# Kernel optimization log

Measured on AMD Instinct MI355X. Metric: run time of the kernel, lower is better.

Reference implementation:

```python
import jax, jax.numpy as jnp
import numpy as np

HIDDEN = 4096
N_HEADS = 32
N_KV_HEADS = 8
HEAD_DIM = HIDDEN // N_HEADS
KV_GROUPS = N_HEADS // N_KV_HEADS
TEMPERATURE = 1.0
NEG_INF = -1e9


def _bitlinear(x, W):
    """BitNet b1.58 BitLinear: per-token int8 activation quant + ternary weight quant (quant-dequant)."""
    # activation: absmax int8 per last dim
    a_scale = 127.0 / jnp.clip(jnp.max(jnp.abs(x), axis=-1, keepdims=True), 1e-5, None)
    xq = jnp.clip(jnp.round(x * a_scale), -128.0, 127.0) / a_scale
    # weight: ternary with mean-abs scale
    w_scale = jnp.clip(jnp.mean(jnp.abs(W)), 1e-5, None)
    Wq = jnp.clip(jnp.round(W / w_scale), -1.0, 1.0) * w_scale
    return jnp.einsum('bsh,oh->bso', xq, Wq)


def _base2_softmax(x, temperature=TEMPERATURE):
    # numerically stable 2^x softmax: 2^((x-m)/T) / sum
    m = jnp.max(x, axis=-1, keepdims=True)
    p = jnp.exp2((x - m) / temperature)
    return p / jnp.sum(p, axis=-1, keepdims=True)


def setup_inputs() -> dict:
    key = jax.random.key(0)
    ks = jax.random.split(key, 6)
    B, S = 2, 2048
    hidden_states = jax.random.normal(ks[0], (B, S, HIDDEN), dtype=jnp.float32)
    # additive causal mask [B, 1, S, S]
    causal = jnp.tril(jnp.ones((S, S), dtype=bool))
    attention_mask = jnp.where(causal, 0.0, NEG_INF).astype(jnp.float32)[None, None]
    attention_mask = jnp.broadcast_to(attention_mask, (B, 1, S, S))
    Wq = jax.random.normal(ks[1], (HIDDEN, HIDDEN), dtype=jnp.float32) * 0.02
    Wk = jax.random.normal(ks[2], (N_KV_HEADS * HEAD_DIM, HIDDEN), dtype=jnp.float32) * 0.02
    Wv = jax.random.normal(ks[3], (N_KV_HEADS * HEAD_DIM, HIDDEN), dtype=jnp.float32) * 0.02
    Wo = jax.random.normal(ks[4], (HIDDEN, HIDDEN), dtype=jnp.float32) * 0.02
    return {"hidden_states": hidden_states, "attention_mask": attention_mask,
            "Wq": Wq, "Wk": Wk, "Wv": Wv, "Wo": Wo}


def reference(hidden_states, attention_mask, Wq, Wk, Wv, Wo):
    B, S, _ = hidden_states.shape
    q = _bitlinear(hidden_states, Wq).reshape(B, S, N_HEADS, HEAD_DIM).transpose(0, 2, 1, 3)
    k = _bitlinear(hidden_states, Wk).reshape(B, S, N_KV_HEADS, HEAD_DIM).transpose(0, 2, 1, 3)
    v = _bitlinear(hidden_states, Wv).reshape(B, S, N_KV_HEADS, HEAD_DIM).transpose(0, 2, 1, 3)
    # GQA: repeat each kv head KV_GROUPS times along head dim
    k = jnp.repeat(k, KV_GROUPS, axis=1)
    v = jnp.repeat(v, KV_GROUPS, axis=1)
    attn_weights = jnp.einsum('bhqd,bhkd->bhqk', q, k) / np.sqrt(HEAD_DIM).astype(np.float32)
    attn_weights = attn_weights + attention_mask
    attn_weights = _base2_softmax(attn_weights)
    attn_output = jnp.einsum('bhqk,bhkd->bhqd', attn_weights, v)
    attn_output = attn_output.transpose(0, 2, 1, 3).reshape(B, S, HIDDEN)
    return _bitlinear(attn_output, Wo)
```

## Files before the change

### kernel.cpp

```cpp
#include <hip/hip_runtime.h>
#include <stdint.h>


typedef float  f32x4 __attribute__((ext_vector_type(4)));
typedef short  s16x8 __attribute__((ext_vector_type(8)));
typedef int    i32x4 __attribute__((ext_vector_type(4)));

__device__ __forceinline__ uint16_t f2b(float f) {
  uint32_t u = __float_as_uint(f);
  return (uint16_t)((u + 0x7FFFu + ((u >> 16) & 1u)) >> 16);
}
__device__ __forceinline__ void gl_lds16(const void* g, void* l) {
  __builtin_amdgcn_global_load_lds((const __attribute__((address_space(1))) unsigned int*)g,
                                   (__attribute__((address_space(3))) unsigned int*)l, 16, 0, 0);
}
__device__ __forceinline__ f32x4 mfma_bf16(s16x8 a, s16x8 b, f32x4 c) {
  return __builtin_amdgcn_mfma_f32_16x16x32_bf16(a, b, c, 0, 0, 0);
}
__device__ __forceinline__ i32x4 mfma_i8(i32x4 a, i32x4 b, i32x4 c) {
  return __builtin_amdgcn_mfma_i32_16x16x64_i8(a, b, c, 0, 0, 0);
}

__global__ __launch_bounds__(256) void k_qact_f32(const float* __restrict__ x,
                                                  int8_t* __restrict__ xq, float* __restrict__ rs) {
  __shared__ float red[4];
  const int row = blockIdx.x, t = threadIdx.x;
  const float4* xr = (const float4*)(x + (size_t)row * 4096);
  float v[16];
  #pragma unroll
  for (int i = 0; i < 4; i++) {
    float4 f = xr[t + 256 * i];
    v[i*4+0] = f.x; v[i*4+1] = f.y; v[i*4+2] = f.z; v[i*4+3] = f.w;
  }
  float mx = 0.f;
  #pragma unroll
  for (int i = 0; i < 16; i++) mx = fmaxf(mx, fabsf(v[i]));
  for (int o = 1; o < 64; o <<= 1) mx = fmaxf(mx, __shfl_xor(mx, o));
  if ((t & 63) == 0) red[t >> 6] = mx;
  __syncthreads();
  mx = fmaxf(fmaxf(red[0], red[1]), fmaxf(red[2], red[3]));
  mx = fmaxf(mx, 1e-5f);
  const float a = 127.f / mx;
  if (t == 0) rs[row] = mx * (1.f / 127.f);
  uint32_t* dst = (uint32_t*)(xq + (size_t)row * 4096);
  #pragma unroll
  for (int i = 0; i < 4; i++) {
    uint32_t w = 0;
    #pragma unroll
    for (int j = 0; j < 4; j++) {
      float q = rintf(v[i*4+j] * a);
      q = fmaxf(-128.f, fminf(127.f, q));
      w |= ((uint32_t)((int)q & 255)) << (j * 8);
    }
    dst[t + 256 * i] = w;
  }
}

__global__ __launch_bounds__(256) void k_abssum_part(const float* __restrict__ wq, const float* __restrict__ wk,
                                                     const float* __restrict__ wv, const float* __restrict__ wo,
                                                     double* __restrict__ part) {
  __shared__ double red[4];
  const int blk = blockIdx.x, t = threadIdx.x;
  const float* src; size_t base;
  if (blk < 1024)      { src = wq; base = (size_t)blk * 16384; }
  else if (blk < 1280) { src = wk; base = (size_t)(blk - 1024) * 16384; }
  else if (blk < 1536) { src = wv; base = (size_t)(blk - 1280) * 16384; }
  else                 { src = wo; base = (size_t)(blk - 1536) * 16384; }
  double s = 0.0;
  #pragma unroll
  for (int r = 0; r < 16; r++) {
    float4 f = *(const float4*)(src + base + r * 1024 + t * 4);
    s += (double)fabsf(f.x) + (double)fabsf(f.y) + (double)fabsf(f.z) + (double)fabsf(f.w);
  }
  for (int o = 1; o < 64; o <<= 1) s += __shfl_xor(s, o);
  if ((t & 63) == 0) red[t >> 6] = s;
  __syncthreads();
  if (t == 0) part[blk] = red[0] + red[1] + red[2] + red[3];
}

__global__ __launch_bounds__(256) void k_reduce_sums(const double* __restrict__ part, double* __restrict__ sums) {
  const int w = threadIdx.x >> 6, lane = threadIdx.x & 63;
  const int s0 = (w == 0) ? 0 : (w == 1) ? 1024 : (w == 2) ? 1280 : 1536;
  const int s1 = (w == 0) ? 1024 : (w == 1) ? 1280 : (w == 2) ? 1536 : 2560;
  double s = 0.0;
  for (int i = s0 + lane; i < s1; i += 64) s += part[i];
  for (int o = 1; o < 64; o <<= 1) s += __shfl_xor(s, o);
  if (lane == 0) sums[w] = s;
}

__global__ __launch_bounds__(256) void k_quant_w_all(const float* __restrict__ wq, const float* __restrict__ wk,
                                                     const float* __restrict__ wv, const float* __restrict__ wo,
                                                     int8_t* __restrict__ wqkv, int8_t* __restrict__ woq,
                                                     const double* __restrict__ sums) {
  const int blk = blockIdx.x, t = threadIdx.x;
  const float* src; int8_t* dst; size_t base; int sidx; double ivn;
  if (blk < 1024)      { src = wq; dst = wqkv;                        base = (size_t)blk * 16384;          sidx = 0; ivn = 1.0 / 16777216.0; }
  else if (blk < 1280) { src = wk; dst = wqkv + (size_t)4096 * 4096;  base = (size_t)(blk - 1024) * 16384; sidx = 1; ivn = 1.0 / 4194304.0;  }
  else if (blk < 1536) { src = wv; dst = wqkv + (size_t)5120 * 4096;  base = (size_t)(blk - 1280) * 16384; sidx = 2; ivn = 1.0 / 4194304.0;  }
  else                 { src = wo; dst = woq;                         base = (size_t)(blk - 1536) * 16384; sidx = 3; ivn = 1.0 / 16777216.0; }
  const float ws = (float)fmax(sums[sidx] * ivn, 1e-5);
  #pragma unroll
  for (int r = 0; r < 16; r++) {
    size_t e = base + r * 1024 + t * 4;
    float4 f = *(const float4*)(src + e);
    float hv[4] = {f.x, f.y, f.z, f.w};
    uint32_t w = 0;
    #pragma unroll
    for (int j = 0; j < 4; j++) {
      float q = rintf(hv[j] / ws);
      q = fmaxf(-1.f, fminf(1.f, q));
      w |= ((uint32_t)((int)q & 255)) << (j * 8);
    }
    *(uint32_t*)(dst + e) = w;
  }
}

template<int MODE>
__global__ __launch_bounds__(256) void k_gemm_i8(const int8_t* __restrict__ A, const int8_t* __restrict__ Bw,
                                                 const float* __restrict__ rs, const double* __restrict__ sums,
                                                 uint16_t* __restrict__ qb, uint16_t* __restrict__ kb,
                                                 uint16_t* __restrict__ vb, float* __restrict__ outp) {
  __shared__ int8_t lA[16384];
  __shared__ int8_t lB[16384];
  const int bn = blockIdx.x, bm = blockIdx.y;
  const int t = threadIdx.x, wave = t >> 6, lane = t & 63;
  const int quad = lane >> 4, l15 = lane & 15;
  const int wm = wave >> 1, wn = wave & 1;

  i32x4 acc[4][4];
  #pragma unroll
  for (int i = 0; i < 4; i++)
    #pragma unroll
    for (int j = 0; j < 4; j++) acc[i][j] = (i32x4){0, 0, 0, 0};

  const size_t arow0 = (size_t)bm * 128;
  const size_t brow0 = (size_t)bn * 128;

  for (int k0 = 0; k0 < 4096; k0 += 128) {
    #pragma unroll
    for (int r = 0; r < 4; r++) {
      int off = r * 4096 + wave * 1024 + lane * 16;
      int row = off >> 7;
      int pos = (off >> 4) & 7;
      int chunk = pos ^ (row & 7);
      gl_lds16(A  + (arow0 + row) * 4096 + k0 + chunk * 16, lA + r * 4096 + wave * 1024);
      gl_lds16(Bw + (brow0 + row) * 4096 + k0 + chunk * 16, lB + r * 4096 + wave * 1024);
    }
    __syncthreads();
    #pragma unroll
    for (int ks = 0; ks < 2; ks++) {
      i32x4 af[4], bf[4];
      #pragma unroll
      for (int i = 0; i < 4; i++) {
        int m = wm * 64 + i * 16 + l15;
        int c = ks * 4 + quad;
        af[i] = *(const i32x4*)(lA + m * 128 + (c ^ (m & 7)) * 16);
        int n = wn * 64 + i * 16 + l15;
        bf[i] = *(const i32x4*)(lB + n * 128 + (c ^ (n & 7)) * 16);
      }
      #pragma unroll
      for (int i = 0; i < 4; i++)
        #pragma unroll
        for (int j = 0; j < 4; j++)
          acc[i][j] = mfma_i8(af[i], bf[j], acc[i][j]);
    }
    __syncthreads();
  }

  float wsc; int sel = 0;
  if (MODE == 0) {
    if (bn < 32)      { wsc = (float)fmax(sums[0] * (1.0 / 16777216.0), 1e-5); sel = 0; }
    else if (bn < 40) { wsc = (float)fmax(sums[1] * (1.0 / 4194304.0),  1e-5); sel = 1; }
    else              { wsc = (float)fmax(sums[2] * (1.0 / 4194304.0),  1e-5); sel = 2; }
  } else {
    wsc = (float)fmax(sums[3] * (1.0 / 16777216.0), 1e-5);
  }
  #pragma unroll
  for (int i = 0; i < 4; i++) {
    #pragma unroll
    for (int r = 0; r < 4; r++) {
      int token = bm * 128 + wm * 64 + i * 16 + quad * 4 + r;
      float rv = rs[token] * wsc;
      #pragma unroll
      for (int j = 0; j < 4; j++) {
        int o = bn * 128 + wn * 64 + j * 16 + l15;
        float val = (float)acc[i][j][r] * rv;
        if (MODE == 0) {
          int b = token >> 11, s2 = token & 2047;
          if (sel == 0) {
            int hh = o >> 7, d = o & 127;
            qb[(((size_t)b * 32 + hh) * 2048 + s2) * 128 + d] = f2b(val * 0.08838834764831845f);
          } else if (sel == 1) {
            int o2 = o - 4096; int g = o2 >> 7, d = o2 & 127;
            kb[(((size_t)b * 8 + g) * 2048 + s2) * 128 + d] = f2b(val);
          } else {
            int o2 = o - 5120; int g = o2 >> 7, d = o2 & 127;
            vb[(((size_t)b * 8 + g) * 2048 + s2) * 128 + d] = f2b(val);
          }
        } else {
          outp[(size_t)token * 4096 + o] = val;
        }
      }
    }
  }
}

__global__ __launch_bounds__(256) void k_transpose_v(const uint16_t* __restrict__ v, uint16_t* __restrict__ vt) {
  __shared__ uint16_t tile[64][72];
  const int bs = blockIdx.x * 64, bd = blockIdx.y * 64, g = blockIdx.z;
  const int t = threadIdx.x;
  const uint16_t* src = v + ((size_t)g * 2048 + bs) * 128 + bd;
  #pragma unroll
  for (int it = 0; it < 2; it++) {
    int r = (t >> 3) + it * 32;
    int c = (t & 7) * 8;
    uint4 u = *(const uint4*)(src + (size_t)r * 128 + c);
    uint16_t* p = &tile[r][c];
    p[0] = u.x & 0xffff; p[1] = u.x >> 16; p[2] = u.y & 0xffff; p[3] = u.y >> 16;
    p[4] = u.z & 0xffff; p[5] = u.z >> 16; p[6] = u.w & 0xffff; p[7] = u.w >> 16;
  }
  __syncthreads();
  uint16_t* dst = vt + ((size_t)g * 128 + bd) * 2048 + bs;
  #pragma unroll
  for (int it = 0; it < 2; it++) {
    int r = (t >> 3) + it * 32;
    int c = (t & 7) * 8;
    uint32_t w0 = tile[c+0][r] | ((uint32_t)tile[c+1][r] << 16);
    uint32_t w1 = tile[c+2][r] | ((uint32_t)tile[c+3][r] << 16);
    uint32_t w2 = tile[c+4][r] | ((uint32_t)tile[c+5][r] << 16);
    uint32_t w3 = tile[c+6][r] | ((uint32_t)tile[c+7][r] << 16);
    *(uint4*)(dst + (size_t)r * 2048 + c) = make_uint4(w0, w1, w2, w3);
  }
}

__global__ __launch_bounds__(256, 4) void k_attn(const uint16_t* __restrict__ qg, const uint16_t* __restrict__ kg,
                                                 const uint16_t* __restrict__ vtg, float* __restrict__ attn) {
  __shared__ char smem[32768];
  const int p = blockIdx.x, bh = blockIdx.y;
  const int b = bh >> 5, h = bh & 31, kv = h >> 2;
  const int t = threadIdx.x, wave = t >> 6, lane = t & 63;
  const int quad = lane >> 4, l15 = lane & 15;

  const char* qbase = (const char*)(qg + (((size_t)b * 32 + h) * 2048) * 128);
  const char* ksrc  = (const char*)(kg + (((size_t)b * 8 + kv) * 2048) * 128);
  const char* vsrc  = (const char*)(vtg + (((size_t)b * 8 + kv) * 128) * 2048);

  for (int pass = 0; pass < 2; pass++) {
    const int qt = pass ? (31 - p) : p;

    __syncthreads();
    #pragma unroll
    for (int r = 0; r < 4; r++) {
      int off = r * 4096 + t * 16;
      int row = off >> 8, pos = (off >> 4) & 15;
      int chunk = pos ^ (row & 7);
      gl_lds16(qbase + (size_t)(qt * 64 + row) * 256 + chunk * 16, smem + off);
    }
    __syncthreads();
    s16x8 qf[4];
    #pragma unroll
    for (int ks = 0; ks < 4; ks++) {
      int n = wave * 16 + l15;
      int c = ks * 4 + quad;
      qf[ks] = *(const s16x8*)(smem + n * 256 + ((c ^ (n & 7))) * 16);
    }

    float Mx = -3.0e38f, Ls = 0.f;
    f32x4 Ov[8];
    #pragma unroll
    for (int mf = 0; mf < 8; mf++) Ov[mf] = (f32x4){0, 0, 0, 0};

    for (int kt = 0; kt <= qt; kt++) {
      __syncthreads();
      #pragma unroll
      for (int r = 0; r < 4; r++) {
        int off = r * 4096 + t * 16;
        { int row = off >> 8, pos = (off >> 4) & 15, chunk = pos ^ (row & 7);
          gl_lds16(ksrc + (size_t)(kt * 64 + row) * 256 + chunk * 16, smem + off); }
        { int row = off >> 7, pos = (off >> 4) & 7, chunk = pos ^ (row & 7);
          gl_lds16(vsrc + (size_t)row * 4096 + kt * 128 + chunk * 16, smem + 16384 + off); }
      }
      __syncthreads();

      f32x4 sc[4];
      #pragma unroll
      for (int mf = 0; mf < 4; mf++) sc[mf] = (f32x4){0, 0, 0, 0};
      #pragma unroll
      for (int ks = 0; ks < 4; ks++) {
        #pragma unroll
        for (int mf = 0; mf < 4; mf++) {
          int m = mf * 16 + l15;
          int c = ks * 4 + quad;
          s16x8 kf = *(const s16x8*)(smem + m * 256 + ((c ^ (m & 7))) * 16);
          sc[mf] = mfma_bf16(kf, qf[ks], sc[mf]);
        }
      }

      if (kt == qt) {
        int qloc = wave * 16 + l15;
        #pragma unroll
        for (int mf = 0; mf < 4; mf++)
          #pragma unroll
          for (int r = 0; r < 4; r++) {
            int kloc = mf * 16 + quad * 4 + r;
            if (kloc > qloc) sc[mf][r] = -3.0e38f;
          }
      }

      float x = sc[0][0];
      #pragma unroll
      for (int mf = 0; mf < 4; mf++)
        #pragma unroll
        for (int r = 0; r < 4; r++) x = fmaxf(x, sc[mf][r]);
      x = fmaxf(x, __shfl_xor(x, 16));
      x = fmaxf(x, __shfl_xor(x, 32));
      float m2 = fmaxf(Mx, x);
      float al = exp2f(Mx - m2);
      Mx = m2;
      float s = 0.f;
      #pragma unroll
      for (int mf = 0; mf < 4; mf++)
        #pragma unroll
        for (int r = 0; r < 4; r++) {
          float pv = exp2f(sc[mf][r] - m2);
          sc[mf][r] = pv;
          s += pv;
        }
      s += __shfl_xor(s, 16);
      s += __shfl_xor(s, 32);
      Ls = Ls * al + s;
      #pragma unroll
      for (int mf = 0; mf < 8; mf++)
        #pragma unroll
        for (int r = 0; r < 4; r++) Ov[mf][r] *= al;

      #pragma unroll
      for (int ks = 0; ks < 2; ks++) {
        uint32_t pk[2][2];
        #pragma unroll
        for (int mfp = 0; mfp < 2; mfp++)
          #pragma unroll
          for (int pr = 0; pr < 2; pr++)
            pk[mfp][pr] = (uint32_t)f2b(sc[2*ks+mfp][2*pr]) |
                          ((uint32_t)f2b(sc[2*ks+mfp][2*pr+1]) << 16);
        uint32_t pf[4];
        #pragma unroll
        for (int j2 = 0; j2 < 4; j2++) {
          int srcLane = ((quad & 1) * 2 + (j2 >> 1)) * 16 + l15;
          uint32_t a0 = __shfl(pk[0][j2 & 1], srcLane);
          uint32_t a1 = __shfl(pk[1][j2 & 1], srcLane);
          pf[j2] = (quad >= 2) ? a1 : a0;
        }
        s16x8 pfr = *(const s16x8*)&pf[0];
        #pragma unroll
        for (int mf = 0; mf < 8; mf++) {
          int m = mf * 16 + l15;
          int c = ks * 4 + quad;
          s16x8 vf = *(const s16x8*)(smem + 16384 + m * 128 + ((c ^ (m & 7))) * 16);
          Ov[mf] = mfma_bf16(vf, pfr, Ov[mf]);
        }
      }
    }

    float inv = 1.f / Ls;
    size_t token = (size_t)b * 2048 + qt * 64 + wave * 16 + l15;
    float* obase = attn + token * 4096 + h * 128 + quad * 4;
    #pragma unroll
    for (int mf = 0; mf < 8; mf++) {
      float4 v4 = make_float4(Ov[mf][0] * inv, Ov[mf][1] * inv, Ov[mf][2] * inv, Ov[mf][3] * inv);
      *(float4*)(obase + mf * 16) = v4;
    }
  }
}

extern "C" void kernel_launch(void* const* d_in, const int* in_sizes, int n_in,
                              void* d_out, int out_size, void* d_ws, size_t ws_size,
                              hipStream_t stream) {
  (void)in_sizes; (void)out_size;
  if (n_in < 6) return;
  const float* hs = (const float*)d_in[0];
  const float* Wq = (const float*)d_in[2];
  const float* Wk = (const float*)d_in[3];
  const float* Wv = (const float*)d_in[4];
  const float* Wo = (const float*)d_in[5];
  float* out = (float*)d_out;

  char* p = (char*)d_ws;
  size_t off = 0;
  auto take = [&](size_t bytes) { char* r = p + off; off += (bytes + 255) & ~(size_t)255; return r; };
  int8_t*   xq1  = (int8_t*)  take((size_t)4096 * 4096);
  float*    rs1  = (float*)   take(4096 * 4);
  int8_t*   wqkv = (int8_t*)  take((size_t)6144 * 4096);
  int8_t*   woq  = (int8_t*)  take((size_t)4096 * 4096);
  uint16_t* qb   = (uint16_t*)take((size_t)2 * 32 * 2048 * 128 * 2);
  uint16_t* kb   = (uint16_t*)take((size_t)2 * 8 * 2048 * 128 * 2);
  uint16_t* vb   = (uint16_t*)take((size_t)2 * 8 * 2048 * 128 * 2);
  uint16_t* vtb  = (uint16_t*)take((size_t)2 * 8 * 2048 * 128 * 2);
  float*    attn = (float*)   take((size_t)4096 * 4096 * 4);
  int8_t*   xq2  = (int8_t*)  take((size_t)4096 * 4096);
  float*    rs2  = (float*)   take(4096 * 4);
  double*   part = (double*)  take(2560 * 8);
  double*   sums = (double*)  take(256);
  if (off > ws_size) return;

  k_abssum_part<<<2560, 256, 0, stream>>>(Wq, Wk, Wv, Wo, part);
  k_reduce_sums<<<1, 256, 0, stream>>>(part, sums);
  k_quant_w_all<<<2560, 256, 0, stream>>>(Wq, Wk, Wv, Wo, wqkv, woq, sums);
  k_qact_f32<<<4096, 256, 0, stream>>>(hs, xq1, rs1);
  k_gemm_i8<0><<<dim3(48, 32), 256, 0, stream>>>(xq1, wqkv, rs1, sums, qb, kb, vb, (float*)nullptr);
  k_transpose_v<<<dim3(32, 2, 16), 256, 0, stream>>>(vb, vtb);
  k_attn<<<dim3(16, 64), 256, 0, stream>>>(qb, kb, vtb, attn);
  k_qact_f32<<<4096, 256, 0, stream>>>(attn, xq2, rs2);
  k_gemm_i8<1><<<dim3(32, 32), 256, 0, stream>>>(xq2, woq, rs2, sums,
                                                 (uint16_t*)nullptr, (uint16_t*)nullptr, (uint16_t*)nullptr, out);
}
```

Baseline: 681.0 us.

## Remap workgroups for XCD locality, add lazy softmax rescale, setprio, packed bf16 cvt

Remaps workgroup IDs in the int8 GEMM and the attention kernel so that consecutive logical tiles land on the same XCD chiplet, which is meant to improve L2 reuse. In attention it skips the online-softmax rescale of O and L unless the running max grows by more than 8 (in log2 units), and wraps the MFMA loops in s_setprio. It also swaps the manual bf16 rounding for the packed v_cvt_pk_bf16_f32 instruction. The lazy rescale lets probabilities reach up to 2^8 before rounding to bf16, which carries an accuracy risk. The remap relies on hardcoded grid sizes.

Result: slower. 731.5 us (+7.4%).

```diff
diff --git a/kernel.cpp b/kernel.cpp
--- a/kernel.cpp
+++ b/kernel.cpp
@@ -9,6 +9,11 @@
 __device__ __forceinline__ uint16_t f2b(float f) {
   uint32_t u = __float_as_uint(f);
   return (uint16_t)((u + 0x7FFFu + ((u >> 16) & 1u)) >> 16);
+}
+__device__ __forceinline__ uint32_t cvt_pk_bf16(float lo, float hi) {
+  uint32_t r;
+  asm("v_cvt_pk_bf16_f32 %0, %1, %2" : "=v"(r) : "v"(lo), "v"(hi));
+  return r;
 }
 __device__ __forceinline__ void gl_lds16(const void* g, void* l) {
   __builtin_amdgcn_global_load_lds((const __attribute__((address_space(1))) unsigned int*)g,
@@ -122,7 +127,12 @@
                                                  uint16_t* __restrict__ vb, float* __restrict__ outp) {
   __shared__ int8_t lA[16384];
   __shared__ int8_t lB[16384];
-  const int bn = blockIdx.x, bm = blockIdx.y;
+  constexpr int NX  = (MODE == 0) ? 48 : 32;
+  constexpr int NWG = NX * 32;
+  constexpr int CH  = NWG / 8;
+  const int wg  = blockIdx.y * NX + blockIdx.x;
+  const int nid = (wg & 7) * CH + (wg >> 3);
+  const int bn = nid >> 5, bm = nid & 31;
   const int t = threadIdx.x, wave = t >> 6, lane = t & 63;
   const int quad = lane >> 4, l15 = lane & 15;
   const int wm = wave >> 1, wn = wave & 1;
@@ -236,7 +246,9 @@
 __global__ __launch_bounds__(256, 4) void k_attn(const uint16_t* __restrict__ qg, const uint16_t* __restrict__ kg,
                                                  const uint16_t* __restrict__ vtg, float* __restrict__ attn) {
   __shared__ char smem[32768];
-  const int p = blockIdx.x, bh = blockIdx.y;
+  const int wg  = blockIdx.y * 16 + blockIdx.x;
+  const int nid = (wg & 7) * 128 + (wg >> 3);
+  const int p = nid & 15, bh = nid >> 4;
   const int b = bh >> 5, h = bh & 31, kv = h >> 2;
   const int t = threadIdx.x, wave = t >> 6, lane = t & 63;
   const int quad = lane >> 4, l15 = lane & 15;
@@ -285,6 +297,7 @@
       f32x4 sc[4];
       #pragma unroll
       for (int mf = 0; mf < 4; mf++) sc[mf] = (f32x4){0, 0, 0, 0};
+      __builtin_amdgcn_s_setprio(1);
       #pragma unroll
       for (int ks = 0; ks < 4; ks++) {
         #pragma unroll
@@ -295,6 +308,7 @@
           sc[mf] = mfma_bf16(kf, qf[ks], sc[mf]);
         }
       }
+      __builtin_amdgcn_s_setprio(0);
 
       if (kt == qt) {
         int qloc = wave * 16 + l15;
@@ -314,25 +328,28 @@
         for (int r = 0; r < 4; r++) x = fmaxf(x, sc[mf][r]);
       x = fmaxf(x, __shfl_xor(x, 16));
       x = fmaxf(x, __shfl_xor(x, 32));
-      float m2 = fmaxf(Mx, x);
-      float al = exp2f(Mx - m2);
-      Mx = m2;
+      if (!__all(x - Mx <= 8.f)) {
+        float m2 = fmaxf(Mx, x);
+        float al = exp2f(Mx - m2);
+        Mx = m2;
+        Ls *= al;
+        #pragma unroll
+        for (int mf = 0; mf < 8; mf++)
+          #pragma unroll
+          for (int r = 0; r < 4; r++) Ov[mf][r] *= al;
+      }
       float s = 0.f;
       #pragma unroll
       for (int mf = 0; mf < 4; mf++)
         #pragma unroll
         for (int r = 0; r < 4; r++) {
-          float pv = exp2f(sc[mf][r] - m2);
+          float pv = exp2f(sc[mf][r] - Mx);
           sc[mf][r] = pv;
           s += pv;
         }
       s += __shfl_xor(s, 16);
       s += __shfl_xor(s, 32);
-      Ls = Ls * al + s;
-      #pragma unroll
-      for (int mf = 0; mf < 8; mf++)
-        #pragma unroll
-        for (int r = 0; r < 4; r++) Ov[mf][r] *= al;
+      Ls += s;
 
       #pragma unroll
       for (int ks = 0; ks < 2; ks++) {
@@ -341,8 +358,7 @@
         for (int mfp = 0; mfp < 2; mfp++)
           #pragma unroll
           for (int pr = 0; pr < 2; pr++)
-            pk[mfp][pr] = (uint32_t)f2b(sc[2*ks+mfp][2*pr]) |
-                          ((uint32_t)f2b(sc[2*ks+mfp][2*pr+1]) << 16);
+            pk[mfp][pr] = cvt_pk_bf16(sc[2*ks+mfp][2*pr], sc[2*ks+mfp][2*pr+1]);
         uint32_t pf[4];
         #pragma unroll
         for (int j2 = 0; j2 < 4; j2++) {
@@ -352,6 +368,7 @@
           pf[j2] = (quad >= 2) ? a1 : a0;
         }
         s16x8 pfr = *(const s16x8*)&pf[0];
+        __builtin_amdgcn_s_setprio(1);
         #pragma unroll
         for (int mf = 0; mf < 8; mf++) {
           int m = mf * 16 + l15;
@@ -359,6 +376,7 @@
           s16x8 vf = *(const s16x8*)(smem + 16384 + m * 128 + ((c ^ (m & 7))) * 16);
           Ov[mf] = mfma_bf16(vf, pfr, Ov[mf]);
         }
+        __builtin_amdgcn_s_setprio(0);
       }
     }
 
```
